# Optimization experiments

Measured on AMD Instinct MI355X. Metric: run time of the kernel, lower is better.

## Reference

```python
import jax, jax.numpy as jnp
import numpy as np

D = 128          # kg_emb_dim
H = 8            # mha_n_heads
N = 20000        # sub-graph nodes per modality
NNZ = 500000     # incidence entries per modality
E = 5000         # hyperedges per modality
C = 50           # context entities
NENT = 50000     # n_entity (rec vocab)


def hyperconv(x, theta, bias, nodes, edges, num_edges):
    # PyG-style HypergraphConv: out = D^-1 H B^-1 H^T (X Theta) + b
    xt = x @ theta                                             # [N, D]
    ones = jnp.ones(nodes.shape[0], xt.dtype)
    e_sum = jax.ops.segment_sum(xt[nodes], edges, num_segments=num_edges)   # [E, D]
    e_deg = jax.ops.segment_sum(ones, edges, num_segments=num_edges)        # [E]
    m = e_sum / jnp.maximum(e_deg, 1.0)[:, None]               # hyperedge means
    n_sum = jax.ops.segment_sum(m[edges], nodes, num_segments=x.shape[0])   # [N, D]
    n_deg = jax.ops.segment_sum(ones, nodes, num_segments=x.shape[0])       # [N]
    return n_sum / jnp.maximum(n_deg, 1.0)[:, None] + bias


def mha(q_x, kv_x, Wq, bq, Wk, bk, Wv, bv, Wo, bo):
    # torch.nn.MultiheadAttention math, batch of 1 (squeezed)
    dh = D // H
    q = (q_x @ Wq + bq).reshape(-1, H, dh)
    k = (kv_x @ Wk + bk).reshape(-1, H, dh)
    v = (kv_x @ Wv + bv).reshape(-1, H, dh)
    scores = jnp.einsum('qhd,khd->hqk', q, k) / jnp.sqrt(jnp.asarray(dh, q.dtype))
    attn = jax.nn.softmax(scores, axis=-1)
    out = jnp.einsum('hqk,khd->qhd', attn, v).reshape(-1, D)
    return out @ Wo + bo


def self_attn(h, a, b):
    # SelfAttentionBatch: softmax(tanh(h a) b) weighted sum over rows
    e = (jnp.tanh(h @ a) @ b)[:, 0]
    return jax.nn.softmax(e) @ h


def setup_inputs() -> dict:
    ks = jax.random.split(jax.random.key(0), 32)
    s = D ** (-0.5)
    inp = {
        'item_emb':   jax.random.normal(ks[0], (N, D), jnp.float32) * s,
        'entity_emb': jax.random.normal(ks[1], (N, D), jnp.float32) * s,
        'word_emb':   jax.random.normal(ks[2], (N, D), jnp.float32) * s,
        'context_entity': jax.random.normal(ks[3], (C, D), jnp.float32) * s,
        'theta_item':   jax.random.normal(ks[4], (D, D), jnp.float32) * s,
        'bias_item':    jax.random.normal(ks[5], (D,), jnp.float32) * 0.02,
        'theta_entity': jax.random.normal(ks[6], (D, D), jnp.float32) * s,
        'bias_entity':  jax.random.normal(ks[7], (D,), jnp.float32) * 0.02,
        'theta_word':   jax.random.normal(ks[8], (D, D), jnp.float32) * s,
        'bias_word':    jax.random.normal(ks[9], (D,), jnp.float32) * 0.02,
        'Wq': jax.random.normal(ks[10], (D, D), jnp.float32) * s,
        'bq': jax.random.normal(ks[11], (D,), jnp.float32) * 0.02,
        'Wk': jax.random.normal(ks[12], (D, D), jnp.float32) * s,
        'bk': jax.random.normal(ks[13], (D,), jnp.float32) * 0.02,
        'Wv': jax.random.normal(ks[14], (D, D), jnp.float32) * s,
        'bv': jax.random.normal(ks[15], (D,), jnp.float32) * 0.02,
        'Wo': jax.random.normal(ks[16], (D, D), jnp.float32) * s,
        'bo': jax.random.normal(ks[17], (D,), jnp.float32) * 0.02,
        'a_his': jax.random.normal(ks[18], (D, D), jnp.float32) * s,
        'b_his': jax.random.normal(ks[19], (D, 1), jnp.float32) * s,
        'a_kg':  jax.random.normal(ks[20], (D, D), jnp.float32) * s,
        'b_kg':  jax.random.normal(ks[21], (D, 1), jnp.float32) * s,
        'rec_W': jax.random.normal(ks[22], (D, NENT), jnp.float32) * s,
        'rec_b': jax.random.normal(ks[23], (NENT,), jnp.float32) * 0.02,
        'item_nodes':   jax.random.randint(ks[24], (NNZ,), 0, N, jnp.int32),
        'item_edges':   jax.random.randint(ks[25], (NNZ,), 0, E, jnp.int32),
        'entity_nodes': jax.random.randint(ks[26], (NNZ,), 0, N, jnp.int32),
        'entity_edges': jax.random.randint(ks[27], (NNZ,), 0, E, jnp.int32),
        'word_nodes':   jax.random.randint(ks[28], (NNZ,), 0, N, jnp.int32),
        'word_edges':   jax.random.randint(ks[29], (NNZ,), 0, E, jnp.int32),
    }
    return inp


def reference(item_emb, entity_emb, word_emb, context_entity,
              theta_item, bias_item, theta_entity, bias_entity, theta_word, bias_word,
              Wq, bq, Wk, bk, Wv, bv, Wo, bo,
              a_his, b_his, a_kg, b_kg, rec_W, rec_b,
              item_nodes, item_edges, entity_nodes, entity_edges, word_nodes, word_edges):
    ih = hyperconv(item_emb, theta_item, bias_item, item_nodes, item_edges, E)
    eh = hyperconv(entity_emb, theta_entity, bias_entity, entity_nodes, entity_edges, E)
    wh = hyperconv(word_emb, theta_word, bias_word, word_nodes, word_edges, E)
    related = jnp.concatenate([ih, eh, wh], axis=0)            # [3N, D]
    # MHItemAttention: context queries attend over related embeddings
    attentive = mha(context_entity, related, Wq, bq, Wk, bk, Wv, bv, Wo, bo)  # [C, D]
    u = self_attn(attentive, a_his, b_his)                     # [D]
    user = jnp.concatenate([context_entity, u[None]], axis=0)  # [C+1, D]
    user_repr = self_attn(user, a_kg, b_kg)                    # [D]
    scores = user_repr @ rec_W + rec_b                         # [NENT]
    return scores
```

## Files before the change

kernel.cpp:

```cpp
#include <hip/hip_runtime.h>
#include <hip/hip_bf16.h>

#define D_ 128
#define H_ 8
#define N_ 20000
#define NNZ_ 500000
#define E_ 5000
#define C_ 50
#define NENT_ 50000
#define NK_ (3*N_)
#define CAPE_ 192
#define CAPN_ 64
#define ENT_PB 4096
#define NBKT 157
#define BCAP 3648
#define ABLK 123
#define NCH3 118
#define KVBLK 235

struct Ptr3f { const float* p[3]; };
struct Ptr3i { const int* p[3]; };
struct GemmB { const float* A[3]; const float* W[3]; unsigned short* C[3]; };

typedef short bf16x8 __attribute__((ext_vector_type(8)));
typedef float f32x4  __attribute__((ext_vector_type(4)));
typedef float f32x2  __attribute__((ext_vector_type(2)));

__device__ __forceinline__ unsigned short f2b(float f){
  unsigned u = __float_as_uint(f);
  u += 0x7FFFu + ((u>>16)&1u);
  return (unsigned short)(u>>16);
}
__device__ __forceinline__ unsigned pk2(float a, float b){
  return (unsigned)f2b(a) | ((unsigned)f2b(b) << 16);
}
__device__ __forceinline__ float blo(unsigned u){ return __uint_as_float(u<<16); }
__device__ __forceinline__ float bhi(unsigned u){ return __uint_as_float(u & 0xFFFF0000u); }

#define GBATCH(SRC, SREG, LBASE) { \
  uint4 uu[8]; \
  _Pragma("unroll") \
  for (int kk=0;kk<8;kk++){ \
    int idx = __shfl(SREG, (LBASE) + 4*kk + rgrp); \
    uu[kk] = *(const uint4*)((SRC) + (size_t)idx*128 + dl*8); \
  } \
  _Pragma("unroll") \
  for (int kk=0;kk<8;kk++){ \
    a01 += (f32x2){blo(uu[kk].x), bhi(uu[kk].x)}; \
    a23 += (f32x2){blo(uu[kk].y), bhi(uu[kk].y)}; \
    a45 += (f32x2){blo(uu[kk].z), bhi(uu[kk].z)}; \
    a67 += (f32x2){blo(uu[kk].w), bhi(uu[kk].w)}; \
  } }

#define PB_PACK 7500
#define PB_Z    7628
#define PB_Q    7629
#define PB_CTX  7693
#define PB_TOT  7743
__global__ __launch_bounds__(256) void prep(Ptr3f xs, unsigned short* __restrict__ xb,
    const float* __restrict__ Wk, const float* __restrict__ Wv, unsigned short* __restrict__ bfB,
    int* __restrict__ gcnt_e, int* __restrict__ gcnt_n, unsigned short* __restrict__ mzero,
    const float* __restrict__ ctx, const float* __restrict__ Wq, const float* __restrict__ bq,
    unsigned short* __restrict__ bfQ,
    const float* __restrict__ a2, const float* __restrict__ b2, float* __restrict__ e2)
{
  int bid = blockIdx.x, t = threadIdx.x;
  if (bid < PB_PACK){
    int mod = bid / 2500, blk = bid - mod*2500;
    int i4 = blk*256 + t;
    float4 v = *(const float4*)(xs.p[mod] + (size_t)i4*4);
    ushort4 o; o.x=f2b(v.x); o.y=f2b(v.y); o.z=f2b(v.z); o.w=f2b(v.w);
    *(ushort4*)(xb + (size_t)mod*N_*D_ + (size_t)i4*4) = o;
  } else if (bid < PB_Z){
    int idx = (bid - PB_PACK)*256 + t;
    int j  = idx & 7;
    int L  = (idx >> 3) & 63;
    int kb = (idx >> 9) & 3;
    int tt = idx >> 11;
    int k = kb*32 + (L>>4)*8 + j;
    int x = L & 15;
    float v = (tt < 8) ? Wk[(size_t)k*128 + tt*16 + x] : Wv[(size_t)k*128 + (tt-8)*16 + x];
    bfB[idx] = f2b(v);
  } else if (bid == PB_Z){
    for (int i=t; i<3*NBKT; i+=256){ gcnt_e[i]=0; gcnt_n[i]=0; }
    if (t < 64)       ((unsigned*)(xb    + (size_t)60000*128))[t]    = 0u;
    else if (t < 128) ((unsigned*)(mzero + (size_t)15000*128))[t-64] = 0u;
  } else if (bid < PB_CTX){
    int idx = (bid - PB_Q)*256 + t;
    int j  = idx & 7;
    int L  = (idx >> 3) & 63;
    int qt = (idx >> 9) & 3;
    int h  = idx >> 11;
    int k  = ((L>>4)&3)*8 + j;
    int q  = qt*16 + (L & 15);
    float val = 0.f;
    if (k < 16 && q < C_){
      const float* cr = ctx + (size_t)q*128;
      const float* wc = Wq + h*16 + k;
      float s0=0.f,s1=0.f,s2=0.f,s3=0.f;
      for (int d=0; d<128; d+=4){
        s0 = fmaf(cr[d],   wc[(size_t) d   *128], s0);
        s1 = fmaf(cr[d+1], wc[(size_t)(d+1)*128], s1);
        s2 = fmaf(cr[d+2], wc[(size_t)(d+2)*128], s2);
        s3 = fmaf(cr[d+3], wc[(size_t)(d+3)*128], s3);
      }
      val = 0.25f * (s0+s1+s2+s3 + bq[h*16+k]);
    }
    bfQ[idx] = f2b(val);
  } else {
    __shared__ float row[128];
    __shared__ float ps[128][2];
    __shared__ float red[2];
    int q = bid - PB_CTX;
    if (t < 128) row[t] = ctx[(size_t)q*128 + t];
    __syncthreads();
    int c = t & 127, half = t >> 7;
    float s = 0.f;
    int d0 = half*64;
    for (int d=d0; d<d0+64; d+=4){
      s = fmaf(row[d],   a2[(size_t) d   *128 + c], s);
      s = fmaf(row[d+1], a2[(size_t)(d+1)*128 + c], s);
      s = fmaf(row[d+2], a2[(size_t)(d+2)*128 + c], s);
      s = fmaf(row[d+3], a2[(size_t)(d+3)*128 + c], s);
    }
    ps[c][half] = s;
    __syncthreads();
    if (t < 128){
      float v = tanhf(ps[t][0] + ps[t][1]) * b2[t];
      #pragma unroll
      for (int k=32; k>=1; k>>=1) v += __shfl_xor(v, k);
      if ((t & 63) == 0) red[t>>6] = v;
    }
    __syncthreads();
    if (t == 0) e2[q] = red[0] + red[1];
  }
}

__global__ __launch_bounds__(256) void binA(Ptr3i nodes, Ptr3i edges,
    unsigned* __restrict__ pe_part, unsigned* __restrict__ pn_part,
    int* __restrict__ gcnt_e, int* __restrict__ gcnt_n)
{
  __shared__ unsigned lbin[ENT_PB];
  __shared__ int cnt[256], off[256];
  __shared__ int gbase[NBKT];
  __shared__ int wsum[4];
  const int mod = blockIdx.y;
  const int* nd = nodes.p[mod];
  const int* ed = edges.p[mod];
  const int base = blockIdx.x * ENT_PB;
  const int t = threadIdx.x;
  const int lane = t & 63, w = t >> 6;

  int myn[16], mye[16], pos[16];
  #pragma unroll
  for (int k=0;k<16;k++){
    int i = base + t + k*256;
    if (i < NNZ_){ myn[k]=nd[i]; mye[k]=ed[i]; }
    else { myn[k]=-1; mye[k]=-1; }
  }

  cnt[t] = 0;
  __syncthreads();
  #pragma unroll
  for (int k=0;k<16;k++)
    if (mye[k] >= 0) pos[k] = atomicAdd(&cnt[mye[k]>>5], 1);
  __syncthreads();
  {
    int v = cnt[t], s = v;
    #pragma unroll
    for (int d=1; d<64; d<<=1){ int u=__shfl_up(s,d); if (lane>=d) s+=u; }
    if (lane==63) wsum[w]=s;
    __syncthreads();
    int wb=0;
    for (int i=0;i<w;i++) wb+=wsum[i];
    off[t] = wb + s - v;
    __syncthreads();
  }
  #pragma unroll
  for (int k=0;k<16;k++)
    if (mye[k] >= 0)
      lbin[off[mye[k]>>5] + pos[k]] = ((unsigned)mye[k] << 15) | (unsigned)myn[k];
  if (t < NBKT && cnt[t] > 0) gbase[t] = atomicAdd(&gcnt_e[mod*NBKT + t], cnt[t]);
  __syncthreads();
  {
    int total = off[255];
    unsigned* dstreg = pe_part + (size_t)mod*NBKT*BCAP;
    for (int i=t; i<total; i+=256){
      unsigned pk = lbin[i];
      int b = pk >> 20;
      int gp = gbase[b] + (i - off[b]);
      if (gp < BCAP) dstreg[(size_t)b*BCAP + gp] = pk;
    }
  }
  __syncthreads();

  cnt[t] = 0;
  __syncthreads();
  #pragma unroll
  for (int k=0;k<16;k++)
    if (myn[k] >= 0) pos[k] = atomicAdd(&cnt[myn[k]>>7], 1);
  __syncthreads();
  {
    int v = cnt[t], s = v;
    #pragma unroll
    for (int d=1; d<64; d<<=1){ int u=__shfl_up(s,d); if (lane>=d) s+=u; }
    if (lane==63) wsum[w]=s;
    __syncthreads();
    int wb=0;
    for (int i=0;i<w;i++) wb+=wsum[i];
    off[t] = wb + s - v;
    __syncthreads();
  }
  #pragma unroll
  for (int k=0;k<16;k++)
    if (myn[k] >= 0)
      lbin[off[myn[k]>>7] + pos[k]] = ((unsigned)myn[k] << 13) | (unsigned)mye[k];
  if (t < NBKT && cnt[t] > 0) gbase[t] = atomicAdd(&gcnt_n[mod*NBKT + t], cnt[t]);
  __syncthreads();
  {
    int total = off[255];
    unsigned* dstreg = pn_part + (size_t)mod*NBKT*BCAP;
    for (int i=t; i<total; i+=256){
      unsigned pk = lbin[i];
      int b = pk >> 20;
      int gp = gbase[b] + (i - off[b]);
      if (gp < BCAP) dstreg[(size_t)b*BCAP + gp] = pk;
    }
  }
}

__global__ __launch_bounds__(256) void binB(const unsigned* __restrict__ pe_part,
    const unsigned* __restrict__ pn_part,
    const int* __restrict__ gcnt_e, const int* __restrict__ gcnt_n,
    int* __restrict__ cnt_all, int* __restrict__ cntA_e,
    unsigned short* __restrict__ e_slot, unsigned short* __restrict__ n_slot)
{
  __shared__ unsigned short ls[128*CAPN_];
  __shared__ int lc[128];
  const int y = blockIdx.y, b = blockIdx.x, t = threadIdx.x;
  if (y < 3){
    const int mod = y;
    {
      unsigned short dmy = (unsigned short)(60000 - mod*20000);
      unsigned dd = (unsigned)dmy * 0x10001u;
      unsigned* lsu32 = (unsigned*)ls;
      for (int i=t; i<32*CAPE_/2; i+=256) lsu32[i] = dd;
    }
    if (t < 64) lc[t] = 0;
    __syncthreads();
    int cnt = gcnt_e[mod*NBKT + b];
    if (cnt > BCAP) cnt = BCAP;
    const unsigned* src = pe_part + ((size_t)mod*NBKT + b)*BCAP;
    for (int i=t; i<cnt; i+=256){
      unsigned pk = src[i];
      int el = (pk >> 15) - b*32;
      int n  = pk & 0x7FFF;
      if (n < (N_>>1)){
        int p = atomicAdd(&lc[el], 1);
        if (p < 96) ls[el*CAPE_ + p] = (unsigned short)n;
      } else {
        int p = atomicAdd(&lc[32 + el], 1);
        if (p < 96) ls[el*CAPE_ + (CAPE_-1 - p)] = (unsigned short)n;
      }
    }
    __syncthreads();
    int rows = E_ - b*32; if (rows > 32) rows = 32;
    if (t < rows){
      cnt_all[mod*(E_+N_) + b*32 + t] = lc[t] + lc[32+t];
      cntA_e[mod*E_ + b*32 + t] = lc[t];
    }
    const unsigned* lsu = (const unsigned*)ls;
    unsigned* dst = (unsigned*)(e_slot + ((size_t)mod*E_ + b*32)*CAPE_);
    int tot = rows*CAPE_/2;
    for (int i=t; i<tot; i+=256) dst[i] = lsu[i];
  } else {
    const int mod = y - 3;
    {
      unsigned short dmy = (unsigned short)(15000 - mod*5000);
      unsigned dd = (unsigned)dmy * 0x10001u;
      unsigned* lsu32 = (unsigned*)ls;
      for (int i=t; i<128*CAPN_/2; i+=256) lsu32[i] = dd;
    }
    if (t < 128) lc[t] = 0;
    __syncthreads();
    int cnt = gcnt_n[mod*NBKT + b];
    if (cnt > BCAP) cnt = BCAP;
    const unsigned* src = pn_part + ((size_t)mod*NBKT + b)*BCAP;
    for (int i=t; i<cnt; i+=256){
      unsigned pk = src[i];
      int nl = (pk >> 13) - b*128;
      int e  = pk & 0x1FFF;
      int p = atomicAdd(&lc[nl], 1);
      if (p < CAPN_) ls[nl*CAPN_ + p] = (unsigned short)e;
    }
    __syncthreads();
    int rows = N_ - b*128; if (rows > 128) rows = 128;
    if (t < rows) cnt_all[mod*(E_+N_) + E_ + b*128 + t] = lc[t];
    const unsigned* lsu = (const unsigned*)ls;
    unsigned* dst = (unsigned*)(n_slot + ((size_t)mod*N_ + b*128)*CAPN_);
    int tot = rows*CAPN_/2;
    for (int i=t; i<tot; i+=256) dst[i] = lsu[i];
  }
}

#define EGB 3752
template<int PHASE>
__global__ __launch_bounds__(256) void e_gather_ph(const unsigned short* __restrict__ xb,
    const int* __restrict__ cnt_all, const int* __restrict__ cntA_e,
    const unsigned short* __restrict__ e_slot, float* __restrict__ m_mean)
{
  const int bid = blockIdx.x;
  const int x = bid & 7, k = bid >> 3;
  int mod, r;
  if (x < 6){
    mod = x / 3;
    int li = x - mod*3;
    int c = 417 - (li == 2);
    if (k < c){
      r = k*3 + li;
    } else {
      int hg = 52*x + (x >= 3) + (k - c);
      mod = 2; r = 938 + hg;
      if (r >= E_/4) return;
    }
  } else {
    mod = 2; r = k*2 + (x - 6);
  }
  const int w = threadIdx.x >> 6, lane = threadIdx.x & 63;
  const int rgrp = lane >> 4, dl = lane & 15;
  const int e = r*4 + w;
  const unsigned short* xt = xb + (size_t)mod*N_*D_;
  int cnt = cnt_all[mod*(E_+N_) + e];
  int cAr = cntA_e[mod*E_ + e];
  int cA = (cAr < 96) ? cAr : 96;
  int cBr = cnt - cAr;
  int cB = (cBr < 96) ? cBr : 96;
  const unsigned short* slot = e_slot + ((size_t)mod*E_ + e)*CAPE_;
  f32x2 a01={0.f,0.f}, a23={0.f,0.f}, a45={0.f,0.f}, a67={0.f,0.f};

  if (PHASE == 0){
    int sv0 = slot[lane], sv1 = slot[64 + lane];
    int cA32 = (cA + 31) & ~31;
    int j = 0;
    int lim0 = (cA32 < 64) ? cA32 : 64;
    for (; j < lim0; j += 32) GBATCH(xt, sv0, j);
    for (; j < cA32; j += 32) GBATCH(xt, sv1, j - 64);
  } else {
    int sv1 = slot[64 + lane], sv2 = slot[128 + lane];
    int cB32 = (cB + 31) & ~31;
    int s0 = CAPE_ - cB32;
    for (int j = s0; j < CAPE_; j += 32){
      if (j < 128) GBATCH(xt, sv1, j - 64)
      else         GBATCH(xt, sv2, j - 128)
    }
  }

  float a0=a01.x, a1=a01.y, a2=a23.x, a3=a23.y, a4=a45.x, a5=a45.y, a6=a67.x, a7=a67.y;
  #pragma unroll
  for (int s=16; s<=32; s<<=1){
    a0 += __shfl_xor(a0, s); a1 += __shfl_xor(a1, s);
    a2 += __shfl_xor(a2, s); a3 += __shfl_xor(a3, s);
    a4 += __shfl_xor(a4, s); a5 += __shfl_xor(a5, s);
    a6 += __shfl_xor(a6, s); a7 += __shfl_xor(a7, s);
  }
  if (rgrp == 0){
    float* dst = m_mean + ((size_t)mod*E_ + e)*128 + dl*8;
    if (PHASE == 0){
      float4 o1; o1.x=a0; o1.y=a1; o1.z=a2; o1.w=a3;
      float4 o2; o2.x=a4; o2.y=a5; o2.z=a6; o2.w=a7;
      *(float4*)dst = o1;
      *(float4*)(dst + 4) = o2;
    } else {
      float inv = 1.f / fmaxf((float)cnt, 1.f);
      float4 o1 = *(const float4*)dst;
      float4 o2 = *(const float4*)(dst + 4);
      o1.x = (o1.x + a0)*inv; o1.y = (o1.y + a1)*inv;
      o1.z = (o1.z + a2)*inv; o1.w = (o1.w + a3)*inv;
      o2.x = (o2.x + a4)*inv; o2.y = (o2.y + a5)*inv;
      o2.z = (o2.z + a6)*inv; o2.w = (o2.w + a7)*inv;
      *(float4*)dst = o1;
      *(float4*)(dst + 4) = o2;
    }
  }
}

__global__ __launch_bounds__(256) void gemm_b(GemmB g, int M)
{
  const float* A = g.A[blockIdx.y];
  const float* W = g.W[blockIdx.y];
  unsigned short* Cout = g.C[blockIdx.y];
  __shared__ float As[64][33];
  __shared__ float Ws[32][128];
  const int t  = threadIdx.x;
  const int br = blockIdx.x * 64;
  const int r0 = (t >> 5) * 8;
  const int c0 = (t & 31) * 4;
  const int lr = t >> 2;
  const int lk = (t & 3) * 8;
  const int wk = t >> 5;

  float acc[8][4];
  #pragma unroll
  for (int i=0;i<8;i++){ acc[i][0]=0.f; acc[i][1]=0.f; acc[i][2]=0.f; acc[i][3]=0.f; }

  for (int kb=0; kb<128; kb+=32){
    float av[8];
    const int grow = br + lr;
    if (grow < M){
      const float* p = A + (size_t)grow*128 + kb + lk;
      float4 a = ((const float4*)p)[0], b = ((const float4*)p)[1];
      av[0]=a.x;av[1]=a.y;av[2]=a.z;av[3]=a.w;av[4]=b.x;av[5]=b.y;av[6]=b.z;av[7]=b.w;
    } else {
      #pragma unroll
      for (int j=0;j<8;j++) av[j]=0.f;
    }
    float4 wv4[4];
    #pragma unroll
    for (int kk=0;kk<4;kk++) wv4[kk] = *(const float4*)&W[(size_t)(kb + wk + kk*8)*128 + c0];

    __syncthreads();
    #pragma unroll
    for (int j=0;j<8;j++) As[lr][lk+j] = av[j];
    #pragma unroll
    for (int kk=0;kk<4;kk++) *(float4*)&Ws[wk + kk*8][c0] = wv4[kk];
    __syncthreads();

    #pragma unroll
    for (int k=0;k<32;k++){
      float4 wv = *(const float4*)&Ws[k][c0];
      #pragma unroll
      for (int i=0;i<8;i++){
        float a = As[r0+i][k];
        acc[i][0] = fmaf(a, wv.x, acc[i][0]);
        acc[i][1] = fmaf(a, wv.y, acc[i][1]);
        acc[i][2] = fmaf(a, wv.z, acc[i][2]);
        acc[i][3] = fmaf(a, wv.w, acc[i][3]);
      }
    }
  }

  #pragma unroll
  for (int i=0;i<8;i++){
    int gr = br + r0 + i;
    if (gr < M){
      ushort4 o;
      o.x=f2b(acc[i][0]); o.y=f2b(acc[i][1]); o.z=f2b(acc[i][2]); o.w=f2b(acc[i][3]);
      *(ushort4*)(Cout + (size_t)gr*128 + c0) = o;
    }
  }
}

__global__ __launch_bounds__(256) void n_gather_w(const unsigned short* __restrict__ m_buf,
    const int* __restrict__ cnt_all, const unsigned short* __restrict__ n_slot,
    Ptr3f biases, unsigned short* __restrict__ relbf)
{
  int mod = blockIdx.y;
  int w = threadIdx.x >> 6, lane = threadIdx.x & 63;
  int rgrp = lane >> 4, dl = lane & 15;
  int n = blockIdx.x*4 + w;
  const unsigned short* m = m_buf + (size_t)mod*E_*D_;
  int cnt = cnt_all[mod*(E_+N_) + E_ + n];
  int c2 = (cnt < CAPN_) ? cnt : CAPN_;
  int c2p = (c2 + 31) & ~31;
  const unsigned short* slot = n_slot + ((size_t)mod*N_ + n)*CAPN_;
  int sv = slot[lane];
  f32x2 a01={0.f,0.f}, a23={0.f,0.f}, a45={0.f,0.f}, a67={0.f,0.f};
  for (int j=0; j<c2p; j+=32) GBATCH(m, sv, j);

  float a0=a01.x, a1=a01.y, a2=a23.x, a3=a23.y, a4=a45.x, a5=a45.y, a6=a67.x, a7=a67.y;
  #pragma unroll
  for (int s=16; s<=32; s<<=1){
    a0 += __shfl_xor(a0, s); a1 += __shfl_xor(a1, s);
    a2 += __shfl_xor(a2, s); a3 += __shfl_xor(a3, s);
    a4 += __shfl_xor(a4, s); a5 += __shfl_xor(a5, s);
    a6 += __shfl_xor(a6, s); a7 += __shfl_xor(a7, s);
  }
  if (rgrp == 0){
    float inv = 1.f / fmaxf((float)cnt, 1.f);
    const float* bs = biases.p[mod] + dl*8;
    uint4 o;
    o.x = pk2(a0*inv + bs[0], a1*inv + bs[1]);
    o.y = pk2(a2*inv + bs[2], a3*inv + bs[3]);
    o.z = pk2(a4*inv + bs[4], a5*inv + bs[5]);
    o.w = pk2(a6*inv + bs[6], a7*inv + bs[7]);
    *(uint4*)(relbf + ((size_t)mod*N_ + n)*128 + dl*8) = o;
  }
}

__global__ __launch_bounds__(256) void gemm_kv_mfma(const unsigned short* __restrict__ relbf,
    const unsigned short* __restrict__ bfB, const float* __restrict__ bk,
    const float* __restrict__ bv, unsigned short* __restrict__ Kb,
    unsigned short* __restrict__ Vtg)
{
  __shared__ unsigned short Bs[32768];
  const int t = threadIdx.x, w = t >> 6, L = t & 63;
  const int m = L & 15, quad = L >> 4, x = m;

  {
    const uint4* src = (const uint4*)bfB;
    uint4* dst = (uint4*)Bs;
    for (int i = t; i < 4096; i += 256) dst[i] = src[i];
  }
  __syncthreads();

  const int rowbase = blockIdx.x*256;
  for (int g = 0; g < 4; g++){
    const int j0 = rowbase + g*64 + w*16;

    bf16x8 a[4];
    {
      int row = j0 + m;
      int rowc = (row < NK_) ? row : (NK_-1);
      #pragma unroll
      for (int kb=0; kb<4; kb++)
        a[kb] = *(const bf16x8*)(relbf + (size_t)rowc*128 + kb*32 + quad*8);
    }

    f32x4 acc[16];
    #pragma unroll
    for (int tt=0; tt<16; tt++) acc[tt] = (f32x4){0.f,0.f,0.f,0.f};

    #pragma unroll
    for (int kb=0; kb<4; kb++){
      #pragma unroll
      for (int tt=0; tt<16; tt++){
        bf16x8 b = *(const bf16x8*)&Bs[(((tt*4 + kb)*64 + L) << 3)];
        acc[tt] = __builtin_amdgcn_mfma_f32_16x16x32_bf16(a[kb], b, acc[tt], 0, 0, 0);
      }
    }

    #pragma unroll
    for (int tt=0; tt<16; tt++){
      int h = tt & 7, kv = tt >> 3;
      float bias = (kv ? bv : bk)[h*16 + x];
      #pragma unroll
      for (int r=0; r<4; r++){
        int jr = j0 + quad*4 + r;
        if (jr < NK_){
          unsigned short val = f2b(acc[tt][r] + bias);
          if (kv == 0) Kb[(((size_t)h*NK_ + jr) << 4) + x] = val;
          else         Vtg[((size_t)(h*16 + x))*NK_ + jr] = val;
        }
      }
    }
  }
}

__global__ __launch_bounds__(256) void flash3(const unsigned short* __restrict__ Kb,
    const unsigned short* __restrict__ Vtg, const unsigned short* __restrict__ bfQ,
    float* __restrict__ part)
{
  __shared__ unsigned short P_lds[4][64][40];
  __shared__ float mbuf[4][64][18];
  const int c = blockIdx.x, h = blockIdx.y;
  const int t = threadIdx.x, w = t >> 6, L = t & 63;
  const int n = L & 15, quad = L >> 4;

  bf16x8 qb[4];
  #pragma unroll
  for (int qt=0; qt<4; qt++)
    qb[qt] = *(const bf16x8*)(bfQ + (((h*4 + qt)*64 + L) << 3));

  float Mc[4], Lc[4];
  f32x4 accq[4];
  #pragma unroll
  for (int qt=0; qt<4; qt++){ Mc[qt] = -INFINITY; Lc[qt] = 0.f; accq[qt] = (f32x4){0.f,0.f,0.f,0.f}; }

  const int base = c*512 + w*128;
  unsigned* Pw = (unsigned*)&P_lds[w][0][0];

  for (int tile=0; tile<4; tile++){
    const int j0 = base + tile*32;
    const bool dead = (j0 >= NK_);

    bf16x8 a0 = (bf16x8){0,0,0,0,0,0,0,0};
    bf16x8 a1 = a0;
    if (quad < 2){
      int k0 = j0 + n;      if (k0 > NK_-1) k0 = NK_-1;
      int k1 = j0 + 16 + n; if (k1 > NK_-1) k1 = NK_-1;
      a0 = *(const bf16x8*)(Kb + (((size_t)h*NK_ + k0) << 4) + quad*8);
      a1 = *(const bf16x8*)(Kb + (((size_t)h*NK_ + k1) << 4) + quad*8);
    }
    f32x4 s0[4], s1[4];
    #pragma unroll
    for (int qt=0; qt<4; qt++){
      s0[qt] = __builtin_amdgcn_mfma_f32_16x16x32_bf16(a0, qb[qt], (f32x4){0.f,0.f,0.f,0.f}, 0,0,0);
      s1[qt] = __builtin_amdgcn_mfma_f32_16x16x32_bf16(a1, qb[qt], (f32x4){0.f,0.f,0.f,0.f}, 0,0,0);
    }

    #pragma unroll
    for (int qt=0; qt<4; qt++){
      float mt = s0[qt][0];
      mt = fmaxf(mt, s0[qt][1]); mt = fmaxf(mt, s0[qt][2]); mt = fmaxf(mt, s0[qt][3]);
      mt = fmaxf(mt, s1[qt][0]); mt = fmaxf(mt, s1[qt][1]);
      mt = fmaxf(mt, s1[qt][2]); mt = fmaxf(mt, s1[qt][3]);
      mt = fmaxf(mt, __shfl_xor(mt, 16));
      mt = fmaxf(mt, __shfl_xor(mt, 32));
      float Mn = fmaxf(Mc[qt], mt);
      float corr = __expf(Mc[qt] - Mn);
      Mc[qt] = Mn;
      float p0[4], p1[4];
      #pragma unroll
      for (int r=0;r<4;r++){
        p0[r] = __expf(s0[qt][r] - Mn);
        p1[r] = __expf(s1[qt][r] - Mn);
      }
      if (dead){
        #pragma unroll
        for (int r=0;r<4;r++){ p0[r]=0.f; p1[r]=0.f; }
      }
      float lt = p0[0]+p0[1]+p0[2]+p0[3]+p1[0]+p1[1]+p1[2]+p1[3];
      lt += __shfl_xor(lt, 16);
      lt += __shfl_xor(lt, 32);
      Lc[qt] = Lc[qt]*corr + lt;
      int rb = (qt*16 + n)*20;
      Pw[rb + quad*2]     = pk2(p0[0], p0[1]);
      Pw[rb + quad*2 + 1] = pk2(p0[2], p0[3]);
      Pw[rb + 8 + quad*2]     = pk2(p1[0], p1[1]);
      Pw[rb + 8 + quad*2 + 1] = pk2(p1[2], p1[3]);
      #pragma unroll
      for (int r=0;r<4;r++){
        float cr = __shfl(corr, quad*4 + r);
        accq[qt][r] *= cr;
      }
    }
    __syncthreads();

    bf16x8 bv_;
    {
      int va = j0 + quad*8; if (va > NK_-8) va = NK_-8;
      bv_ = *(const bf16x8*)(Vtg + ((size_t)(h*16 + n))*NK_ + va);
    }
    #pragma unroll
    for (int qt=0; qt<4; qt++){
      bf16x8 pa = *(const bf16x8*)&P_lds[w][qt*16 + n][quad*8];
      accq[qt] = __builtin_amdgcn_mfma_f32_16x16x32_bf16(pa, bv_, accq[qt], 0,0,0);
    }
    __syncthreads();
  }

  #pragma unroll
  for (int qt=0; qt<4; qt++){
    #pragma unroll
    for (int r=0; r<4; r++)
      mbuf[w][qt*16 + quad*4 + r][2 + n] = accq[qt][r];
    if (quad == 0){
      mbuf[w][qt*16 + n][0] = Mc[qt];
      mbuf[w][qt*16 + n][1] = Lc[qt];
    }
  }
  __syncthreads();
  if (t < C_){
    float M = mbuf[0][t][0], Lm = mbuf[0][t][1];
    float A[16];
    #pragma unroll
    for (int i=0;i<16;i++) A[i] = mbuf[0][t][2+i];
    #pragma unroll
    for (int ww=1; ww<4; ww++){
      float pm = mbuf[ww][t][0], pl = mbuf[ww][t][1];
      if (pl > 0.f){
        float mn = fmaxf(M, pm);
        float c1 = __expf(M - mn), c2 = __expf(pm - mn);
        Lm = Lm*c1 + pl*c2;
        #pragma unroll
        for (int i=0;i<16;i++) A[i] = A[i]*c1 + mbuf[ww][t][2+i]*c2;
        M = mn;
      }
    }
    float* pp = part + ((size_t)(h*NCH3 + c)*C_ + t)*18;
    pp[0] = M; pp[1] = Lm;
    #pragma unroll
    for (int i=0;i<16;i++) pp[2+i] = A[i];
  }
}

__global__ __launch_bounds__(512) void merge_oproj_e1(const float* __restrict__ part,
    const float* __restrict__ Wo, const float* __restrict__ bo,
    const float* __restrict__ a1, const float* __restrict__ b1,
    float* __restrict__ attentive, float* __restrict__ e1)
{
  __shared__ float row[128];
  __shared__ float ps[128][4];
  __shared__ float orow[128];
  __shared__ float red[2];
  const int q = blockIdx.x, t = threadIdx.x;
  const int h = t >> 6, lane = t & 63;

  {
    float M = -1e30f, L = 0.f;
    float A[16];
    #pragma unroll
    for (int i=0;i<16;i++) A[i] = 0.f;

    #pragma unroll
    for (int cc=0; cc<2; cc++){
      int c = lane + cc*64;
      if (c < NCH3){
        const float* p = part + ((size_t)(h*NCH3 + c)*C_ + q)*18;
        float pm = p[0], pl = p[1];
        if (pl > 0.f){
          float Mn = fmaxf(M, pm);
          float w1 = __expf(M - Mn), w2 = __expf(pm - Mn);
          L = L*w1 + pl*w2;
          #pragma unroll
          for (int i=0;i<16;i++) A[i] = fmaf(A[i], w1, p[2+i]*w2);
          M = Mn;
        }
      }
    }
    #pragma unroll
    for (int d=32; d>=1; d>>=1){
      float pm = __shfl_xor(M, d);
      float pl = __shfl_xor(L, d);
      float Ao[16];
      #pragma unroll
      for (int i=0;i<16;i++) Ao[i] = __shfl_xor(A[i], d);
      float Mn = fmaxf(M, pm);
      float w1 = __expf(M - Mn), w2 = __expf(pm - Mn);
      L = L*w1 + pl*w2;
      #pragma unroll
      for (int i=0;i<16;i++) A[i] = fmaf(A[i], w1, Ao[i]*w2);
      M = Mn;
    }
    if (lane == 0){
      float invL = 1.f / L;
      #pragma unroll
      for (int i=0;i<16;i++) row[h*16 + i] = A[i]*invL;
    }
  }
  __syncthreads();

  const int c = t & 127, seg = t >> 7;
  {
    float s = 0.f;
    int d0 = seg*32;
    for (int d=d0; d<d0+32; d+=4){
      s = fmaf(row[d],   Wo[(size_t) d   *128 + c], s);
      s = fmaf(row[d+1], Wo[(size_t)(d+1)*128 + c], s);
      s = fmaf(row[d+2], Wo[(size_t)(d+2)*128 + c], s);
      s = fmaf(row[d+3], Wo[(size_t)(d+3)*128 + c], s);
    }
    ps[c][seg] = s;
  }
  __syncthreads();
  if (t < 128){
    float o = ps[t][0]+ps[t][1]+ps[t][2]+ps[t][3] + bo[t];
    attentive[(size_t)q*128 + t] = o;
    orow[t] = o;
  }
  __syncthreads();
  {
    float s = 0.f;
    int d0 = seg*32;
    for (int d=d0; d<d0+32; d+=4){
      s = fmaf(orow[d],   a1[(size_t) d   *128 + c], s);
      s = fmaf(orow[d+1], a1[(size_t)(d+1)*128 + c], s);
      s = fmaf(orow[d+2], a1[(size_t)(d+2)*128 + c], s);
      s = fmaf(orow[d+3], a1[(size_t)(d+3)*128 + c], s);
    }
    ps[c][seg] = s;
  }
  __syncthreads();
  if (t < 128){
    float v = tanhf(ps[t][0]+ps[t][1]+ps[t][2]+ps[t][3]) * b1[t];
    #pragma unroll
    for (int k=32; k>=1; k>>=1) v += __shfl_xor(v, k);
    if ((t & 63) == 0) red[t>>6] = v;
  }
  __syncthreads();
  if (t == 0) e1[q] = red[0] + red[1];
}

__global__ __launch_bounds__(128) void tail_mid(const float* __restrict__ attentive,
    const float* __restrict__ ctx, const float* __restrict__ a2, const float* __restrict__ b2,
    const float* __restrict__ e1, const float* __restrict__ e2, float* __restrict__ user_repr)
{
  __shared__ float p[64];
  __shared__ float u[128];
  __shared__ float red[2];
  __shared__ float p2[64];
  const int t = threadIdx.x;

  if (t == 0){
    float mx=-INFINITY;
    for (int i=0;i<C_;i++) mx=fmaxf(mx,e1[i]);
    float ss=0.f;
    for (int i=0;i<C_;i++){ p[i]=__expf(e1[i]-mx); ss+=p[i]; }
    float inv=1.f/ss;
    for (int i=0;i<C_;i++) p[i]*=inv;
  }
  __syncthreads();
  {
    float s=0.f;
    for (int r=0;r<C_;r++) s = fmaf(p[r], attentive[(size_t)r*128 + t], s);
    u[t] = s;
  }
  __syncthreads();
  {
    float s0=0.f,s1=0.f,s2=0.f,s3=0.f;
    for (int d=0; d<128; d+=4){
      s0 = fmaf(u[d],   a2[(size_t) d   *128 + t], s0);
      s1 = fmaf(u[d+1], a2[(size_t)(d+1)*128 + t], s1);
      s2 = fmaf(u[d+2], a2[(size_t)(d+2)*128 + t], s2);
      s3 = fmaf(u[d+3], a2[(size_t)(d+3)*128 + t], s3);
    }
    float v = tanhf(s0+s1+s2+s3) * b2[t];
    #pragma unroll
    for (int k=32; k>=1; k>>=1) v += __shfl_xor(v, k);
    if ((t & 63) == 0) red[t>>6] = v;
  }
  __syncthreads();
  if (t == 0){
    float elast = red[0] + red[1];
    float mx=elast;
    for (int i=0;i<C_;i++) mx=fmaxf(mx,e2[i]);
    float ss=0.f;
    for (int i=0;i<C_;i++){ p2[i]=__expf(e2[i]-mx); ss+=p2[i]; }
    float pl = __expf(elast-mx); ss += pl;
    float inv=1.f/ss;
    for (int i=0;i<C_;i++) p2[i]*=inv;
    p2[C_] = pl*inv;
  }
  __syncthreads();
  {
    float s=0.f;
    for (int r=0;r<C_;r++) s = fmaf(p2[r], ctx[(size_t)r*128 + t], s);
    s = fmaf(p2[C_], u[t], s);
    user_repr[t] = s;
  }
}

__global__ __launch_bounds__(256) void scores_k(const float* __restrict__ ur,
    const float* __restrict__ recW, const float* __restrict__ recb, float* __restrict__ out)
{
  __shared__ float u[128];
  int t = threadIdx.x;
  if (t < 128) u[t] = ur[t];
  __syncthreads();
  int j = blockIdx.x*256 + t;
  if (j < NENT_){
    float s0=0.f,s1=0.f,s2=0.f,s3=0.f;
    for (int d=0; d<128; d+=4){
      s0 = fmaf(u[d],   recW[(size_t) d   *NENT_ + j], s0);
      s1 = fmaf(u[d+1], recW[(size_t)(d+1)*NENT_ + j], s1);
      s2 = fmaf(u[d+2], recW[(size_t)(d+2)*NENT_ + j], s2);
      s3 = fmaf(u[d+3], recW[(size_t)(d+3)*NENT_ + j], s3);
    }
    out[j] = s0+s1+s2+s3 + recb[j];
  }
}

extern "C" void kernel_launch(void* const* d_in, const int* in_sizes, int n_in,
                              void* d_out, int out_size, void* d_ws, size_t ws_size,
                              hipStream_t stream)
{
  auto f32 = [&](int i){ return (const float*)d_in[i]; };
  Ptr3i nodes = {{(const int*)d_in[24], (const int*)d_in[26], (const int*)d_in[28]}};
  Ptr3i edges = {{(const int*)d_in[25], (const int*)d_in[27], (const int*)d_in[29]}};

  char* base = (char*)d_ws;
  int*   cnt_all = (int*)base;
  int*   gcnt_e  = (int*)(base + 300064);
  int*   gcnt_n  = gcnt_e + NBKT*3;
  unsigned short* n_slot = (unsigned short*)(base + 300064 + 4096);
  float* m_mean  = (float*)((char*)n_slot + 7680000);
  unsigned short* m_buf = (unsigned short*)((char*)m_mean + 7680000);
  unsigned short* relbf = (unsigned short*)((char*)m_buf + 3840256);
  unsigned short* bfB   = (unsigned short*)((char*)relbf + 15360000);
  unsigned short* bfQ   = (unsigned short*)((char*)bfB + 65536);
  float* attentive = (float*)((char*)bfQ + 32768);
  float* user_repr = (float*)((char*)attentive + 25600);
  float* e1buf     = user_repr + 128;
  float* e2buf     = e1buf + 64;
  int*   cntA_e    = (int*)(e2buf + 64);
  float* fpart = (float*)relbf;
  char* U = (char*)(cntA_e + 3*E_);
  unsigned* pe_part = (unsigned*)U;
  unsigned* pn_part = pe_part + (size_t)3*NBKT*BCAP;
  unsigned short* e_slot = (unsigned short*)(pn_part + (size_t)3*NBKT*BCAP);
  unsigned short* xb     = e_slot + (size_t)3*E_*CAPE_;
  unsigned short* Kb  = (unsigned short*)U;
  unsigned short* Vtg = Kb + (size_t)H_*NK_*16;

  Ptr3f xs = {{f32(0), f32(1), f32(2)}};
  prep<<<PB_TOT, 256, 0, stream>>>(xs, xb, f32(12), f32(14), bfB, gcnt_e, gcnt_n, m_buf,
                                   f32(3), f32(10), f32(11), bfQ, f32(20), f32(21), e2buf);

  binA<<<dim3(ABLK, 3), 256, 0, stream>>>(nodes, edges, pe_part, pn_part, gcnt_e, gcnt_n);
  binB<<<dim3(NBKT, 6), 256, 0, stream>>>(pe_part, pn_part, gcnt_e, gcnt_n, cnt_all, cntA_e,
                                          e_slot, n_slot);

  e_gather_ph<0><<<EGB, 256, 0, stream>>>(xb, cnt_all, cntA_e, e_slot, m_mean);
  e_gather_ph<1><<<EGB, 256, 0, stream>>>(xb, cnt_all, cntA_e, e_slot, m_mean);
  GemmB g;
  for (int mod=0; mod<3; mod++){
    g.A[mod] = m_mean + (size_t)mod*E_*D_;
    g.W[mod] = f32(4 + 2*mod);
    g.C[mod] = m_buf + (size_t)mod*E_*D_;
  }
  gemm_b<<<dim3((E_+63)/64, 3), 256, 0, stream>>>(g, E_);
  Ptr3f biases = {{f32(5), f32(7), f32(9)}};
  n_gather_w<<<dim3(N_/4, 3), 256, 0, stream>>>(m_buf, cnt_all, n_slot, biases, relbf);

  gemm_kv_mfma<<<KVBLK, 256, 0, stream>>>(relbf, bfB, f32(13), f32(15), Kb, Vtg);
  flash3<<<dim3(NCH3, H_), 256, 0, stream>>>(Kb, Vtg, bfQ, fpart);
  merge_oproj_e1<<<C_, 512, 0, stream>>>(fpart, f32(16), f32(17), f32(18), f32(19),
                                         attentive, e1buf);

  tail_mid<<<1, 128, 0, stream>>>(attentive, f32(3), f32(20), f32(21), e1buf, e2buf, user_repr);
  scores_k<<<(NENT_+255)/256, 256, 0, stream>>>(user_repr, f32(22), f32(23), (float*)d_out);
}
```

Baseline: 336.1 us.

## Merge two-phase edge gather into one pass and fuse tail into scores kernel

Drops the node-index half split in edge binning, so each hyperedge's slot is filled linearly and a single gather kernel sums all members and writes the mean. This removes one kernel launch and the read-modify-write of the m_mean buffer. The single-block tail_mid is folded into scores_k, and every scores block now recomputes the small user representation redundantly in exchange for one fewer launch and serial step. The gather loops are also unrolled into fixed guarded batches. The split was likely there for cache locality over halves of the node table, which the single pass gives up.

```diff
diff --git a/kernel.cpp b/kernel.cpp
--- a/kernel.cpp
+++ b/kernel.cpp
@@ -232,7 +232,7 @@
 __global__ __launch_bounds__(256) void binB(const unsigned* __restrict__ pe_part,
     const unsigned* __restrict__ pn_part,
     const int* __restrict__ gcnt_e, const int* __restrict__ gcnt_n,
-    int* __restrict__ cnt_all, int* __restrict__ cntA_e,
+    int* __restrict__ cnt_all,
     unsigned short* __restrict__ e_slot, unsigned short* __restrict__ n_slot)
 {
   __shared__ unsigned short ls[128*CAPN_];
@@ -246,7 +246,7 @@
       unsigned* lsu32 = (unsigned*)ls;
       for (int i=t; i<32*CAPE_/2; i+=256) lsu32[i] = dd;
     }
-    if (t < 64) lc[t] = 0;
+    if (t < 32) lc[t] = 0;
     __syncthreads();
     int cnt = gcnt_e[mod*NBKT + b];
     if (cnt > BCAP) cnt = BCAP;
@@ -255,20 +255,12 @@
       unsigned pk = src[i];
       int el = (pk >> 15) - b*32;
       int n  = pk & 0x7FFF;
-      if (n < (N_>>1)){
-        int p = atomicAdd(&lc[el], 1);
-        if (p < 96) ls[el*CAPE_ + p] = (unsigned short)n;
-      } else {
-        int p = atomicAdd(&lc[32 + el], 1);
-        if (p < 96) ls[el*CAPE_ + (CAPE_-1 - p)] = (unsigned short)n;
-      }
+      int p = atomicAdd(&lc[el], 1);
+      if (p < CAPE_) ls[el*CAPE_ + p] = (unsigned short)n;
     }
     __syncthreads();
     int rows = E_ - b*32; if (rows > 32) rows = 32;
-    if (t < rows){
-      cnt_all[mod*(E_+N_) + b*32 + t] = lc[t] + lc[32+t];
-      cntA_e[mod*E_ + b*32 + t] = lc[t];
-    }
+    if (t < rows) cnt_all[mod*(E_+N_) + b*32 + t] = lc[t];
     const unsigned* lsu = (const unsigned*)ls;
     unsigned* dst = (unsigned*)(e_slot + ((size_t)mod*E_ + b*32)*CAPE_);
     int tot = rows*CAPE_/2;
@@ -304,10 +296,9 @@
 }
 
 #define EGB 3752
-template<int PHASE>
-__global__ __launch_bounds__(256) void e_gather_ph(const unsigned short* __restrict__ xb,
-    const int* __restrict__ cnt_all, const int* __restrict__ cntA_e,
-    const unsigned short* __restrict__ e_slot, float* __restrict__ m_mean)
+__global__ __launch_bounds__(256) void e_gather_w(const unsigned short* __restrict__ xb,
+    const int* __restrict__ cnt_all, const unsigned short* __restrict__ e_slot,
+    float* __restrict__ m_mean)
 {
   const int bid = blockIdx.x;
   const int x = bid & 7, k = bid >> 3;
@@ -331,29 +322,18 @@
   const int e = r*4 + w;
   const unsigned short* xt = xb + (size_t)mod*N_*D_;
   int cnt = cnt_all[mod*(E_+N_) + e];
-  int cAr = cntA_e[mod*E_ + e];
-  int cA = (cAr < 96) ? cAr : 96;
-  int cBr = cnt - cAr;
-  int cB = (cBr < 96) ? cBr : 96;
+  int c2 = (cnt < CAPE_) ? cnt : CAPE_;
+  int c2p = (c2 + 31) & ~31;
   const unsigned short* slot = e_slot + ((size_t)mod*E_ + e)*CAPE_;
+  int sv0 = slot[lane], sv1 = slot[64 + lane], sv2 = slot[128 + lane];
   f32x2 a01={0.f,0.f}, a23={0.f,0.f}, a45={0.f,0.f}, a67={0.f,0.f};
 
-  if (PHASE == 0){
-    int sv0 = slot[lane], sv1 = slot[64 + lane];
-    int cA32 = (cA + 31) & ~31;
-    int j = 0;
-    int lim0 = (cA32 < 64) ? cA32 : 64;
-    for (; j < lim0; j += 32) GBATCH(xt, sv0, j);
-    for (; j < cA32; j += 32) GBATCH(xt, sv1, j - 64);
-  } else {
-    int sv1 = slot[64 + lane], sv2 = slot[128 + lane];
-    int cB32 = (cB + 31) & ~31;
-    int s0 = CAPE_ - cB32;
-    for (int j = s0; j < CAPE_; j += 32){
-      if (j < 128) GBATCH(xt, sv1, j - 64)
-      else         GBATCH(xt, sv2, j - 128)
-    }
-  }
+  if (c2p > 0)   GBATCH(xt, sv0, 0);
+  if (c2p > 32)  GBATCH(xt, sv0, 32);
+  if (c2p > 64)  GBATCH(xt, sv1, 0);
+  if (c2p > 96)  GBATCH(xt, sv1, 32);
+  if (c2p > 128) GBATCH(xt, sv2, 0);
+  if (c2p > 160) GBATCH(xt, sv2, 32);
 
   float a0=a01.x, a1=a01.y, a2=a23.x, a3=a23.y, a4=a45.x, a5=a45.y, a6=a67.x, a7=a67.y;
   #pragma unroll
@@ -364,23 +344,12 @@
     a6 += __shfl_xor(a6, s); a7 += __shfl_xor(a7, s);
   }
   if (rgrp == 0){
+    float inv = 1.f / fmaxf((float)cnt, 1.f);
     float* dst = m_mean + ((size_t)mod*E_ + e)*128 + dl*8;
-    if (PHASE == 0){
-      float4 o1; o1.x=a0; o1.y=a1; o1.z=a2; o1.w=a3;
-      float4 o2; o2.x=a4; o2.y=a5; o2.z=a6; o2.w=a7;
-      *(float4*)dst = o1;
-      *(float4*)(dst + 4) = o2;
-    } else {
-      float inv = 1.f / fmaxf((float)cnt, 1.f);
-      float4 o1 = *(const float4*)dst;
-      float4 o2 = *(const float4*)(dst + 4);
-      o1.x = (o1.x + a0)*inv; o1.y = (o1.y + a1)*inv;
-      o1.z = (o1.z + a2)*inv; o1.w = (o1.w + a3)*inv;
-      o2.x = (o2.x + a4)*inv; o2.y = (o2.y + a5)*inv;
-      o2.z = (o2.z + a6)*inv; o2.w = (o2.w + a7)*inv;
-      *(float4*)dst = o1;
-      *(float4*)(dst + 4) = o2;
-    }
+    float4 o1; o1.x=a0*inv; o1.y=a1*inv; o1.z=a2*inv; o1.w=a3*inv;
+    float4 o2; o2.x=a4*inv; o2.y=a5*inv; o2.z=a6*inv; o2.w=a7*inv;
+    *(float4*)dst = o1;
+    *(float4*)(dst + 4) = o2;
   }
 }
 
@@ -465,7 +434,8 @@
   const unsigned short* slot = n_slot + ((size_t)mod*N_ + n)*CAPN_;
   int sv = slot[lane];
   f32x2 a01={0.f,0.f}, a23={0.f,0.f}, a45={0.f,0.f}, a67={0.f,0.f};
-  for (int j=0; j<c2p; j+=32) GBATCH(m, sv, j);
+  if (c2p > 0)  GBATCH(m, sv, 0);
+  if (c2p > 32) GBATCH(m, sv, 32);
 
   float a0=a01.x, a1=a01.y, a2=a23.x, a3=a23.y, a4=a45.x, a5=a45.y, a6=a67.x, a7=a67.y;
   #pragma unroll
@@ -771,14 +741,16 @@
   if (t == 0) e1[q] = red[0] + red[1];
 }
 
-__global__ __launch_bounds__(128) void tail_mid(const float* __restrict__ attentive,
+__global__ __launch_bounds__(256) void tail_scores(const float* __restrict__ attentive,
     const float* __restrict__ ctx, const float* __restrict__ a2, const float* __restrict__ b2,
-    const float* __restrict__ e1, const float* __restrict__ e2, float* __restrict__ user_repr)
+    const float* __restrict__ e1, const float* __restrict__ e2,
+    const float* __restrict__ recW, const float* __restrict__ recb, float* __restrict__ out)
 {
   __shared__ float p[64];
   __shared__ float u[128];
   __shared__ float red[2];
   __shared__ float p2[64];
+  __shared__ float ur[128];
   const int t = threadIdx.x;
 
   if (t == 0){
@@ -790,13 +762,13 @@
     for (int i=0;i<C_;i++) p[i]*=inv;
   }
   __syncthreads();
-  {
+  if (t < 128){
     float s=0.f;
     for (int r=0;r<C_;r++) s = fmaf(p[r], attentive[(size_t)r*128 + t], s);
     u[t] = s;
   }
   __syncthreads();
-  {
+  if (t < 128){
     float s0=0.f,s1=0.f,s2=0.f,s3=0.f;
     for (int d=0; d<128; d+=4){
       s0 = fmaf(u[d],   a2[(size_t) d   *128 + t], s0);
@@ -822,29 +794,21 @@
     p2[C_] = pl*inv;
   }
   __syncthreads();
-  {
+  if (t < 128){
     float s=0.f;
     for (int r=0;r<C_;r++) s = fmaf(p2[r], ctx[(size_t)r*128 + t], s);
     s = fmaf(p2[C_], u[t], s);
-    user_repr[t] = s;
-  }
-}
-
-__global__ __launch_bounds__(256) void scores_k(const float* __restrict__ ur,
-    const float* __restrict__ recW, const float* __restrict__ recb, float* __restrict__ out)
-{
-  __shared__ float u[128];
-  int t = threadIdx.x;
-  if (t < 128) u[t] = ur[t];
+    ur[t] = s;
+  }
   __syncthreads();
   int j = blockIdx.x*256 + t;
   if (j < NENT_){
     float s0=0.f,s1=0.f,s2=0.f,s3=0.f;
     for (int d=0; d<128; d+=4){
-      s0 = fmaf(u[d],   recW[(size_t) d   *NENT_ + j], s0);
-      s1 = fmaf(u[d+1], recW[(size_t)(d+1)*NENT_ + j], s1);
-      s2 = fmaf(u[d+2], recW[(size_t)(d+2)*NENT_ + j], s2);
-      s3 = fmaf(u[d+3], recW[(size_t)(d+3)*NENT_ + j], s3);
+      s0 = fmaf(ur[d],   recW[(size_t) d   *NENT_ + j], s0);
+      s1 = fmaf(ur[d+1], recW[(size_t)(d+1)*NENT_ + j], s1);
+      s2 = fmaf(ur[d+2], recW[(size_t)(d+2)*NENT_ + j], s2);
+      s3 = fmaf(ur[d+3], recW[(size_t)(d+3)*NENT_ + j], s3);
     }
     out[j] = s0+s1+s2+s3 + recb[j];
   }
@@ -872,9 +836,8 @@
   float* user_repr = (float*)((char*)attentive + 25600);
   float* e1buf     = user_repr + 128;
   float* e2buf     = e1buf + 64;
-  int*   cntA_e    = (int*)(e2buf + 64);
   float* fpart = (float*)relbf;
-  char* U = (char*)(cntA_e + 3*E_);
+  char* U = (char*)(e2buf + 64);
   unsigned* pe_part = (unsigned*)U;
   unsigned* pn_part = pe_part + (size_t)3*NBKT*BCAP;
   unsigned short* e_slot = (unsigned short*)(pn_part + (size_t)3*NBKT*BCAP);
@@ -887,11 +850,10 @@
                                    f32(3), f32(10), f32(11), bfQ, f32(20), f32(21), e2buf);
 
   binA<<<dim3(ABLK, 3), 256, 0, stream>>>(nodes, edges, pe_part, pn_part, gcnt_e, gcnt_n);
-  binB<<<dim3(NBKT, 6), 256, 0, stream>>>(pe_part, pn_part, gcnt_e, gcnt_n, cnt_all, cntA_e,
+  binB<<<dim3(NBKT, 6), 256, 0, stream>>>(pe_part, pn_part, gcnt_e, gcnt_n, cnt_all,
                                           e_slot, n_slot);
 
-  e_gather_ph<0><<<EGB, 256, 0, stream>>>(xb, cnt_all, cntA_e, e_slot, m_mean);
-  e_gather_ph<1><<<EGB, 256, 0, stream>>>(xb, cnt_all, cntA_e, e_slot, m_mean);
+  e_gather_w<<<EGB, 256, 0, stream>>>(xb, cnt_all, e_slot, m_mean);
   GemmB g;
   for (int mod=0; mod<3; mod++){
     g.A[mod] = m_mean + (size_t)mod*E_*D_;
@@ -907,6 +869,6 @@
   merge_oproj_e1<<<C_, 512, 0, stream>>>(fpart, f32(16), f32(17), f32(18), f32(19),
                                          attentive, e1buf);
 
-  tail_mid<<<1, 128, 0, stream>>>(attentive, f32(3), f32(20), f32(21), e1buf, e2buf, user_repr);
-  scores_k<<<(NENT_+255)/256, 256, 0, stream>>>(user_repr, f32(22), f32(23), (float*)d_out);
-}
+  tail_scores<<<(NENT_+255)/256, 256, 0, stream>>>(attentive, f32(3), f32(20), f32(21),
+                                                   e1buf, e2buf, f32(22), f32(23), (float*)d_out);
+}
```

Result: no change. 336.2 us (+0.0%).
